# Kernel tuning notes

Hardware: AMD Instinct MI355X
Metric: run time of the kernel (lower is better)

## Reference

```python
import jax, jax.numpy as jnp
import numpy as np

DIM_X, DIM_Z, D_MODEL, N_HEADS, BATCH = 512, 256, 256, 8, 32


def sinusoidal_pe(seq_len, d_model):
    # standard sinusoidal table, rows indexed by position
    pos = np.arange(seq_len)[:, None].astype(np.float32)
    div = np.exp(np.arange(0, d_model, 2).astype(np.float32) * (-np.log(10000.0) / d_model))
    pe = np.zeros((seq_len, d_model), dtype=np.float32)
    pe[:, 0::2] = np.sin(pos * div)
    pe[:, 1::2] = np.cos(pos * div)
    return jnp.asarray(pe)


def setup_inputs() -> dict:
    key = jax.random.key(0)
    ks = jax.random.split(key, 5)
    state = jax.random.normal(ks[0], (BATCH, D_MODEL, DIM_X), dtype=jnp.float32)
    obs = jax.random.normal(ks[1], (BATCH, D_MODEL, DIM_Z), dtype=jnp.float32)
    Qp = jax.random.uniform(ks[2], (DIM_X, D_MODEL), dtype=jnp.float32)  # torch.rand init
    Wq = jax.random.normal(ks[3], (D_MODEL, D_MODEL), dtype=jnp.float32) / np.sqrt(D_MODEL)
    Wk = jax.random.normal(ks[4], (D_MODEL, D_MODEL), dtype=jnp.float32) / np.sqrt(D_MODEL)
    bq = jnp.zeros((D_MODEL,), dtype=jnp.float32)
    bk = jnp.zeros((D_MODEL,), dtype=jnp.float32)
    return {"state": state, "obs": obs, "Qp": Qp, "Wq": Wq, "bq": bq, "Wk": Wk, "bk": bk}


def reference(state, obs, Qp, Wq, bq, Wk, bk):
    bs, en, dim_x = state.shape
    dim_z = obs.shape[2]
    d_model = Qp.shape[1]
    h = N_HEADS
    hd = d_model // h
    S = dim_x + dim_z

    # mean-center over the ensemble axis
    A = state - jnp.mean(state, axis=1, keepdims=True)   # [bs, en, dim_x]
    Y = obs - jnp.mean(obs, axis=1, keepdims=True)       # [bs, en, dim_z]
    A = jnp.transpose(A, (2, 0, 1))                      # [dim_x, bs, en]
    Y = jnp.transpose(Y, (2, 0, 1))                      # [dim_z, bs, en]

    # positional encoding: batch_first=True quirk -> PE indexed along axis 1 (the bs axis)
    pe = sinusoidal_pe(bs, d_model)[None, :, :]          # [1, bs, d_model]
    query = Qp[:, None, :] + pe                          # [dim_x, bs, d_model] (broadcast of repeat)
    xy = jnp.concatenate([A, Y], axis=0) + pe            # [S, bs, d_model]

    # multi-head attention weights (V / out-proj do not affect returned quantities)
    q = (query @ Wq.T + bq).reshape(dim_x, bs, h, hd)
    k = (xy @ Wk.T + bk).reshape(S, bs, h, hd)
    scores = jnp.einsum('lbhd,sbhd->bhls', q, k) / np.sqrt(hd)  # [bs, h, dim_x, S]

    # fixed structured mask: eye(dim_x) | bottom-padded eye(dim_z)
    p1 = jnp.eye(dim_x, dtype=bool)
    p2 = jnp.concatenate([jnp.zeros((dim_x - dim_z, dim_z), dtype=bool),
                          jnp.eye(dim_z, dtype=bool)], axis=0)
    allow = jnp.concatenate([p1, p2], axis=1)            # [dim_x, S]
    scores = jnp.where(allow[None, None], scores, -jnp.inf)
    atten = jnp.mean(jax.nn.softmax(scores, axis=-1), axis=1)  # average over heads -> [bs, dim_x, S]

    # weighted merge of the ORIGINAL (uncentered) state/obs
    merge = jnp.concatenate([jnp.transpose(state, (0, 2, 1)),
                             jnp.transpose(obs, (0, 2, 1))], axis=1)  # [bs, S, en]
    new_state = jnp.einsum('bls,bse->ble', atten, merge)              # [bs, dim_x, en]
    new_state = jnp.transpose(new_state, (0, 2, 1))                   # [bs, en, dim_x]
    return new_state, atten
```

## Files before the change

kernel.cpp:

```cpp
#include <hip/hip_runtime.h>
#include <stdint.h>
#include <math.h>


#define WS_P    0
#define WS_QWT  8192
#define WS_PQ   73728
#define WS_U    81920
#define WS_V    606208
#define WS_QPT  671744
#define WS_WQT  737280

typedef float vf4 __attribute__((ext_vector_type(4)));
__device__ __forceinline__ void nt_store4(float* p, float x, float y,
                                          float z, float w) {
  vf4 v; v.x = x; v.y = y; v.z = z; v.w = w;
  __builtin_nontemporal_store(v, (vf4*)p);
}

__global__ void __launch_bounds__(256)
k_tr(const float* __restrict__ Qp, const float* __restrict__ Wq,
     float* __restrict__ ws, float* __restrict__ out) {
  int bid = blockIdx.x, t = threadIdx.x;
  if (bid < 128) {
    __shared__ float tile[32][33];
    const float* src; float* dst; int ti;
    if (bid < 64) { src = Qp + 65536; dst = ws + WS_QPT; ti = bid; }
    else          { src = Wq;         dst = ws + WS_WQT; ti = bid - 64; }
    int tr = ti >> 3, tc = ti & 7;
    int c = t & 31, r0 = t >> 5;
    #pragma unroll
    for (int k = 0; k < 4; ++k) {
      int r = r0 + (k << 3);
      tile[r][c] = src[(size_t)(tr * 32 + r) * 256 + tc * 32 + c];
    }
    __syncthreads();
    #pragma unroll
    for (int k = 0; k < 4; ++k) {
      int r = r0 + (k << 3);
      dst[(size_t)(tc * 32 + r) * 256 + tr * 32 + c] = tile[c][r];
    }
  } else {
    int base = (bid - 128) * 512 + t;
    #pragma unroll
    for (int k = 0; k < 2; ++k) {
      int g4 = base + (k << 8);
      int row_id = g4 / 192, c = g4 - row_id * 192;
      int b = row_id >> 8, l = row_id & 255;
      float v[4] = {0.f, 0.f, 0.f, 0.f};
      int s0 = c << 2;
      if (l >= s0 && l < s0 + 4) v[l - s0] = 1.0f;
      nt_store4(out + 4194304 + (size_t)((b << 9) + l) * 768 + (c << 2),
                v[0], v[1], v[2], v[3]);
    }
  }
}

__global__ void __launch_bounds__(256)
k_pro(const float* __restrict__ Wq, float* __restrict__ ws,
      float* __restrict__ out) {
  int bid = blockIdx.x, t = threadIdx.x;
  if (bid < 288) {
    __shared__ float lvec[256];
    const float* __restrict__ GT; float* dst;
    if (bid < 256) {
      int d = bid;
      lvec[t] = Wq[(size_t)d * 256 + t];
      GT = ws + WS_QPT; dst = ws + WS_QWT + d * 256;
    } else {
      int b = bid - 256;
      int k2 = t & ~1;
      float div = expf((float)k2 * (-9.210340371976184f / 256.f));
      float a = (float)b * div;
      lvec[t] = (t & 1) ? cosf(a) : sinf(a);
      GT = ws + WS_WQT; dst = ws + WS_PQ + b * 256;
    }
    __syncthreads();
    float acc = 0.f;
    #pragma unroll 8
    for (int e = 0; e < 256; ++e)
      acc += lvec[e] * GT[(e << 8) + t];
    dst[t] = acc;
  } else {
    int base = (bid - 288) * 512 + t;
    #pragma unroll
    for (int k = 0; k < 2; ++k) {
      int g4 = base + (k << 8);
      int row_id = g4 / 192, c = g4 - row_id * 192;
      int b = row_id >> 8, l = 256 + (row_id & 255);
      nt_store4(out + 4194304 + (size_t)((b << 9) + l) * 768 + (c << 2),
                0.f, 0.f, 0.f, 0.f);
    }
  }
}

__global__ void __launch_bounds__(256)
k_uv(const float* __restrict__ Wk, const float* __restrict__ bq,
     const float* __restrict__ state, float* __restrict__ ws,
     float* __restrict__ out) {
  int bid = blockIdx.x, t = threadIdx.x;
  if (bid < 256) {
    int h = bid >> 5, e0 = (bid & 31) << 3;
    __shared__ float wk_s[32][9];
    {
      int d = t >> 3, i = t & 7;
      wk_s[d][i] = Wk[(size_t)(h * 32 + d) * 256 + e0 + i];
    }
    __syncthreads();
    float acc[8] = {0.f, 0.f, 0.f, 0.f, 0.f, 0.f, 0.f, 0.f};
    const float* __restrict__ Qw = ws + WS_QWT + t;
    #pragma unroll 4
    for (int d = 0; d < 32; ++d) {
      float q = Qw[((h << 5) + d) << 8];
      #pragma unroll
      for (int i = 0; i < 8; ++i) acc[i] += wk_s[d][i] * q;
    }
    float* Uh = ws + WS_U + (h << 16) + (size_t)e0 * 256;
    #pragma unroll
    for (int i = 0; i < 8; ++i) Uh[(size_t)i * 256 + t] = acc[i];
  } else if (bid < 512) {
    int idx = bid - 256, b = idx >> 3, h = idx & 7;
    float acc = 0.f;
#pragma unroll 8
    for (int dd = 0; dd < 32; ++dd) {
      int d = h * 32 + dd;
      acc += (ws[WS_PQ + b * 256 + d] + bq[d]) * Wk[(size_t)d * 256 + t];
    }
    ws[WS_V + ((b << 3) + h) * 256 + t] = acc;
  } else {
    int base = (bid - 512) * 512 + t;
    #pragma unroll
    for (int k = 0; k < 2; ++k) {
      int g4 = base + (k << 8);
      int row = g4 >> 6, c = g4 & 63;
      float4 sv = ((const float4*)state)[(size_t)row * 128 + c];
      nt_store4(out + (size_t)row * 512 + (c << 2), sv.x, sv.y, sv.z, sv.w);
    }
  }
}

__global__ void __launch_bounds__(256)
k_delta(const float* __restrict__ state, const float* __restrict__ obs,
        float* __restrict__ ws) {
  int b = blockIdx.x >> 3, jt = (blockIdx.x & 7) << 5;
  int t = threadIdx.x;
  __shared__ float Xs[256][33];
  __shared__ float Vs[2048];
  __shared__ float pd[8][8][32];
  __shared__ float pw[8][8][32];
  __shared__ float px[8][32];
  {
    int es = t >> 3, jq = t & 7;
    const float* sp = state + (size_t)b * 131072 + 256 + jt + (jq << 2);
    const float* op = obs   + (size_t)b * 65536  + jt + (jq << 2);
    #pragma unroll
    for (int k = 0; k < 8; ++k) {
      int e = es + (k << 5);
      float4 s4 = *(const float4*)(sp + (size_t)e * 512);
      float4 o4 = *(const float4*)(op + (size_t)e * 256);
      float* xr = &Xs[e][jq << 2];
      xr[0] = s4.x - o4.x; xr[1] = s4.y - o4.y;
      xr[2] = s4.z - o4.z; xr[3] = s4.w - o4.w;
    }
    for (int i = t; i < 2048; i += 256) Vs[i] = ws[WS_V + (b << 11) + i];
  }
  __syncthreads();
  int j = t & 31, eg = t >> 5, e0 = eg << 5;
  {
    float ax = 0.f;
    #pragma unroll
    for (int ei = 0; ei < 32; ++ei) ax += Xs[e0 + ei][j];
    px[eg][j] = ax;
  }
  const float* __restrict__ Ub = ws + WS_U + jt + j;
  #pragma unroll
  for (int h = 0; h < 8; ++h) {
    float dacc = 0.f, wacc = 0.f;
    const float* __restrict__ Uh = Ub + (h << 16) + (e0 << 8);
    const float* __restrict__ Vh = Vs + (h << 8) + e0;
    #pragma unroll 16
    for (int ei = 0; ei < 32; ++ei) {
      float w = Uh[ei << 8] + Vh[ei];
      dacc += Xs[e0 + ei][j] * w;
      wacc += w;
    }
    pd[eg][h][j] = dacc;
    pw[eg][h][j] = wacc;
  }
  __syncthreads();
  int h2 = t >> 5, j2 = t & 31;
  float D = 0.f, W = 0.f, X = 0.f;
  #pragma unroll
  for (int g = 0; g < 8; ++g) {
    D += pd[g][h2][j2];
    W += pw[g][h2][j2];
    X += px[g][j2];
  }
  float delta = D - X * (1.f / 256.f) * W;
  float sig = 1.f / (1.f + __expf(-delta * 0.17677669529663687f));
  __syncthreads();
  px[h2][j2] = sig;
  __syncthreads();
  if (t < 32) {
    float acc = 0.f;
    #pragma unroll
    for (int h = 0; h < 8; ++h) acc += px[h][t];
    ws[WS_P + (b << 8) + jt + t] = acc;
  }
}

__global__ void __launch_bounds__(256)
k_out(const float* __restrict__ state, const float* __restrict__ obs,
      const float* __restrict__ ws, float* __restrict__ out) {
  int bid = blockIdx.x, t = threadIdx.x;
  if (bid < 2048) {
    int row = (bid << 2) | (t >> 6);
    int c = t & 63;
    int b = row >> 8;
    float4 sv = ((const float4*)(state + (size_t)row * 512))[64 + c];
    float4 ov = ((const float4*)(obs + (size_t)row * 256))[c];
    float4 p4 = ((const float4*)(ws + WS_P + b * 256))[c];
    p4.x *= 0.125f; p4.y *= 0.125f; p4.z *= 0.125f; p4.w *= 0.125f;
    nt_store4(out + (size_t)row * 512 + 256 + (c << 2),
              p4.x * sv.x + (1.f - p4.x) * ov.x,
              p4.y * sv.y + (1.f - p4.y) * ov.y,
              p4.z * sv.z + (1.f - p4.z) * ov.z,
              p4.w * sv.w + (1.f - p4.w) * ov.w);
  } else {
    int idx = ((bid - 2048) << 8) + t;
    int b = idx >> 8, j = idx & 255;
    float p = ws[WS_P + (b << 8) + j] * 0.125f;
    size_t r = 4194304 + (size_t)((b << 9) + 256 + j) * 768;
    out[r + 256 + j] = p;
    out[r + 512 + j] = 1.f - p;
  }
}

extern "C" void kernel_launch(void* const* d_in, const int* in_sizes, int n_in,
                              void* d_out, int out_size, void* d_ws, size_t ws_size,
                              hipStream_t stream) {
  const float *state = nullptr, *obs = nullptr, *Qp = nullptr;
  const float *Wq = nullptr, *Wk = nullptr, *bq = nullptr, *bk = nullptr;
  for (int i = 0; i < n_in; ++i) {
    int s = in_sizes[i];
    const float* p = (const float*)d_in[i];
    if      (s == 4194304) state = p;
    else if (s == 2097152) obs = p;
    else if (s == 131072)  Qp = p;
    else if (s == 65536)   { if (!Wq) Wq = p; else Wk = p; }
    else if (s == 256)     { if (!bq) bq = p; else bk = p; }
  }
  (void)bk;
  float* out = (float*)d_out;
  float* ws  = (float*)d_ws;

  k_tr   <<<3200, 256, 0, stream>>>(Qp, Wq, ws, out);
  k_pro  <<<3360, 256, 0, stream>>>(Wq, ws, out);
  k_uv   <<<1536, 256, 0, stream>>>(Wk, bq, state, ws, out);
  k_delta<<<256,  256, 0, stream>>>(state, obs, ws);
  k_out  <<<2080, 256, 0, stream>>>(state, obs, ws, out);
}
```

Baseline: 126.7 us.

## Fuse five kernels into one cooperative persistent kernel with grid syncs

Replaces the five separate launches with a single cooperative kernel of 512 blocks that runs the phases in order, separated by grid-wide barriers. The static output writes (identity, zeros and the state copy) are redistributed as grid-stride loops across the phases, so they overlap with the small compute blocks. The aim is to remove launch gaps and per-kernel tail effects. In exchange it adds four grid.sync barriers, limits parallelism to 512 resident blocks, and uses about 58KB of shared memory per block, which may affect occupancy.

```diff
diff --git a/kernel.cpp b/kernel.cpp
--- a/kernel.cpp
+++ b/kernel.cpp
@@ -1,6 +1,9 @@
 #include <hip/hip_runtime.h>
+#include <hip/hip_cooperative_groups.h>
 #include <stdint.h>
 #include <math.h>
+
+namespace cg = cooperative_groups;
 
 
 #define WS_P    0
@@ -18,12 +21,42 @@
   __builtin_nontemporal_store(v, (vf4*)p);
 }
 
-__global__ void __launch_bounds__(256)
-k_tr(const float* __restrict__ Qp, const float* __restrict__ Wq,
+__device__ __forceinline__ void write_static(int idx, const float* __restrict__ state,
+                                             float* __restrict__ out) {
+  if (idx < 1572864) {
+    int g4 = idx;
+    int row_id = g4 / 192, c = g4 - row_id * 192;
+    int b = row_id >> 8, l = row_id & 255;
+    float v[4] = {0.f, 0.f, 0.f, 0.f};
+    int s0 = c << 2;
+    if (l >= s0 && l < s0 + 4) v[l - s0] = 1.0f;
+    nt_store4(out + 4194304 + (size_t)((b << 9) + l) * 768 + (c << 2),
+              v[0], v[1], v[2], v[3]);
+  } else if (idx < 3145728) {
+    int g4 = idx - 1572864;
+    int row_id = g4 / 192, c = g4 - row_id * 192;
+    int b = row_id >> 8, l = 256 + (row_id & 255);
+    nt_store4(out + 4194304 + (size_t)((b << 9) + l) * 768 + (c << 2),
+              0.f, 0.f, 0.f, 0.f);
+  } else {
+    int g4 = idx - 3145728;
+    int row = g4 >> 6, c = g4 & 63;
+    float4 sv = ((const float4*)state)[(size_t)row * 128 + c];
+    nt_store4(out + (size_t)row * 512 + (c << 2), sv.x, sv.y, sv.z, sv.w);
+  }
+}
+
+__global__ void __launch_bounds__(256, 2)
+mega(const float* __restrict__ state, const float* __restrict__ obs,
+     const float* __restrict__ Qp, const float* __restrict__ Wq,
+     const float* __restrict__ Wk, const float* __restrict__ bq,
      float* __restrict__ ws, float* __restrict__ out) {
+  cg::grid_group grid = cg::this_grid();
+  __shared__ float S[14848];
   int bid = blockIdx.x, t = threadIdx.x;
+
   if (bid < 128) {
-    __shared__ float tile[32][33];
+    float (*tile)[33] = (float(*)[33])S;
     const float* src; float* dst; int ti;
     if (bid < 64) { src = Qp + 65536; dst = ws + WS_QPT; ti = bid; }
     else          { src = Wq;         dst = ws + WS_WQT; ti = bid - 64; }
@@ -41,27 +74,13 @@
       dst[(size_t)(tc * 32 + r) * 256 + tr * 32 + c] = tile[c][r];
     }
   } else {
-    int base = (bid - 128) * 512 + t;
-    #pragma unroll
-    for (int k = 0; k < 2; ++k) {
-      int g4 = base + (k << 8);
-      int row_id = g4 / 192, c = g4 - row_id * 192;
-      int b = row_id >> 8, l = row_id & 255;
-      float v[4] = {0.f, 0.f, 0.f, 0.f};
-      int s0 = c << 2;
-      if (l >= s0 && l < s0 + 4) v[l - s0] = 1.0f;
-      nt_store4(out + 4194304 + (size_t)((b << 9) + l) * 768 + (c << 2),
-                v[0], v[1], v[2], v[3]);
-    }
-  }
-}
-
-__global__ void __launch_bounds__(256)
-k_pro(const float* __restrict__ Wq, float* __restrict__ ws,
-      float* __restrict__ out) {
-  int bid = blockIdx.x, t = threadIdx.x;
+    for (int i = ((bid - 128) << 8) + t; i < 1433600; i += 98304)
+      write_static(i, state, out);
+  }
+  grid.sync();
+
   if (bid < 288) {
-    __shared__ float lvec[256];
+    float* lvec = S;
     const float* __restrict__ GT; float* dst;
     if (bid < 256) {
       int d = bid;
@@ -82,29 +101,17 @@
       acc += lvec[e] * GT[(e << 8) + t];
     dst[t] = acc;
   } else {
-    int base = (bid - 288) * 512 + t;
-    #pragma unroll
-    for (int k = 0; k < 2; ++k) {
-      int g4 = base + (k << 8);
-      int row_id = g4 / 192, c = g4 - row_id * 192;
-      int b = row_id >> 8, l = 256 + (row_id & 255);
-      nt_store4(out + 4194304 + (size_t)((b << 9) + l) * 768 + (c << 2),
-                0.f, 0.f, 0.f, 0.f);
-    }
-  }
-}
-
-__global__ void __launch_bounds__(256)
-k_uv(const float* __restrict__ Wk, const float* __restrict__ bq,
-     const float* __restrict__ state, float* __restrict__ ws,
-     float* __restrict__ out) {
-  int bid = blockIdx.x, t = threadIdx.x;
+    for (int i = 1433600 + ((bid - 288) << 8) + t; i < 2662400; i += 57344)
+      write_static(i, state, out);
+  }
+  grid.sync();
+
   if (bid < 256) {
     int h = bid >> 5, e0 = (bid & 31) << 3;
-    __shared__ float wk_s[32][9];
+    float* wk_s = S;
     {
       int d = t >> 3, i = t & 7;
-      wk_s[d][i] = Wk[(size_t)(h * 32 + d) * 256 + e0 + i];
+      wk_s[d * 9 + i] = Wk[(size_t)(h * 32 + d) * 256 + e0 + i];
     }
     __syncthreads();
     float acc[8] = {0.f, 0.f, 0.f, 0.f, 0.f, 0.f, 0.f, 0.f};
@@ -113,109 +120,98 @@
     for (int d = 0; d < 32; ++d) {
       float q = Qw[((h << 5) + d) << 8];
       #pragma unroll
-      for (int i = 0; i < 8; ++i) acc[i] += wk_s[d][i] * q;
+      for (int i = 0; i < 8; ++i) acc[i] += wk_s[d * 9 + i] * q;
     }
     float* Uh = ws + WS_U + (h << 16) + (size_t)e0 * 256;
     #pragma unroll
     for (int i = 0; i < 8; ++i) Uh[(size_t)i * 256 + t] = acc[i];
-  } else if (bid < 512) {
+  } else {
     int idx = bid - 256, b = idx >> 3, h = idx & 7;
     float acc = 0.f;
-#pragma unroll 8
+    #pragma unroll 8
     for (int dd = 0; dd < 32; ++dd) {
       int d = h * 32 + dd;
       acc += (ws[WS_PQ + b * 256 + d] + bq[d]) * Wk[(size_t)d * 256 + t];
     }
     ws[WS_V + ((b << 3) + h) * 256 + t] = acc;
-  } else {
-    int base = (bid - 512) * 512 + t;
-    #pragma unroll
-    for (int k = 0; k < 2; ++k) {
-      int g4 = base + (k << 8);
-      int row = g4 >> 6, c = g4 & 63;
-      float4 sv = ((const float4*)state)[(size_t)row * 128 + c];
-      nt_store4(out + (size_t)row * 512 + (c << 2), sv.x, sv.y, sv.z, sv.w);
-    }
-  }
-}
-
-__global__ void __launch_bounds__(256)
-k_delta(const float* __restrict__ state, const float* __restrict__ obs,
-        float* __restrict__ ws) {
-  int b = blockIdx.x >> 3, jt = (blockIdx.x & 7) << 5;
-  int t = threadIdx.x;
-  __shared__ float Xs[256][33];
-  __shared__ float Vs[2048];
-  __shared__ float pd[8][8][32];
-  __shared__ float pw[8][8][32];
-  __shared__ float px[8][32];
-  {
-    int es = t >> 3, jq = t & 7;
-    const float* sp = state + (size_t)b * 131072 + 256 + jt + (jq << 2);
-    const float* op = obs   + (size_t)b * 65536  + jt + (jq << 2);
-    #pragma unroll
-    for (int k = 0; k < 8; ++k) {
-      int e = es + (k << 5);
-      float4 s4 = *(const float4*)(sp + (size_t)e * 512);
-      float4 o4 = *(const float4*)(op + (size_t)e * 256);
-      float* xr = &Xs[e][jq << 2];
-      xr[0] = s4.x - o4.x; xr[1] = s4.y - o4.y;
-      xr[2] = s4.z - o4.z; xr[3] = s4.w - o4.w;
-    }
-    for (int i = t; i < 2048; i += 256) Vs[i] = ws[WS_V + (b << 11) + i];
-  }
-  __syncthreads();
-  int j = t & 31, eg = t >> 5, e0 = eg << 5;
-  {
-    float ax = 0.f;
-    #pragma unroll
-    for (int ei = 0; ei < 32; ++ei) ax += Xs[e0 + ei][j];
-    px[eg][j] = ax;
-  }
-  const float* __restrict__ Ub = ws + WS_U + jt + j;
+  }
+  grid.sync();
+
+  if (bid < 256) {
+    int b = bid >> 3, jt = (bid & 7) << 5;
+    float* Xs = S;
+    float* Vs = S + 8448;
+    float* pd = S + 10496;
+    float* pw = S + 12544;
+    float* px = S + 14592;
+    {
+      int es = t >> 3, jq = t & 7;
+      const float* sp = state + (size_t)b * 131072 + 256 + jt + (jq << 2);
+      const float* op = obs   + (size_t)b * 65536  + jt + (jq << 2);
+      #pragma unroll
+      for (int k = 0; k < 8; ++k) {
+        int e = es + (k << 5);
+        float4 s4 = *(const float4*)(sp + (size_t)e * 512);
+        float4 o4 = *(const float4*)(op + (size_t)e * 256);
+        float* xr = Xs + e * 33 + (jq << 2);
+        xr[0] = s4.x - o4.x; xr[1] = s4.y - o4.y;
+        xr[2] = s4.z - o4.z; xr[3] = s4.w - o4.w;
+      }
+      for (int i = t; i < 2048; i += 256) Vs[i] = ws[WS_V + (b << 11) + i];
+    }
+    __syncthreads();
+    int j = t & 31, eg = t >> 5, e0 = eg << 5;
+    {
+      float ax = 0.f;
+      #pragma unroll
+      for (int ei = 0; ei < 32; ++ei) ax += Xs[(e0 + ei) * 33 + j];
+      px[eg * 32 + j] = ax;
+    }
+    const float* __restrict__ Ub = ws + WS_U + jt + j;
+    #pragma unroll
+    for (int h = 0; h < 8; ++h) {
+      float dacc = 0.f, wacc = 0.f;
+      const float* __restrict__ Uh = Ub + (h << 16) + (e0 << 8);
+      const float* __restrict__ Vh = Vs + (h << 8) + e0;
+      #pragma unroll 16
+      for (int ei = 0; ei < 32; ++ei) {
+        float w = Uh[ei << 8] + Vh[ei];
+        dacc += Xs[(e0 + ei) * 33 + j] * w;
+        wacc += w;
+      }
+      pd[((eg << 3) + h) * 32 + j] = dacc;
+      pw[((eg << 3) + h) * 32 + j] = wacc;
+    }
+    __syncthreads();
+    int h2 = t >> 5, j2 = t & 31;
+    float D = 0.f, W = 0.f, X = 0.f;
+    #pragma unroll
+    for (int g = 0; g < 8; ++g) {
+      D += pd[((g << 3) + h2) * 32 + j2];
+      W += pw[((g << 3) + h2) * 32 + j2];
+      X += px[g * 32 + j2];
+    }
+    float delta = D - X * (1.f / 256.f) * W;
+    float sig = 1.f / (1.f + __expf(-delta * 0.17677669529663687f));
+    __syncthreads();
+    px[h2 * 32 + j2] = sig;
+    __syncthreads();
+    if (t < 32) {
+      float acc = 0.f;
+      #pragma unroll
+      for (int h = 0; h < 8; ++h) acc += px[h * 32 + t];
+      ws[WS_P + (b << 8) + jt + t] = acc;
+    }
+  } else {
+    for (int i = 2662400 + ((bid - 256) << 8) + t; i < 3670016; i += 65536)
+      write_static(i, state, out);
+  }
+  grid.sync();
+
   #pragma unroll
-  for (int h = 0; h < 8; ++h) {
-    float dacc = 0.f, wacc = 0.f;
-    const float* __restrict__ Uh = Ub + (h << 16) + (e0 << 8);
-    const float* __restrict__ Vh = Vs + (h << 8) + e0;
-    #pragma unroll 16
-    for (int ei = 0; ei < 32; ++ei) {
-      float w = Uh[ei << 8] + Vh[ei];
-      dacc += Xs[e0 + ei][j] * w;
-      wacc += w;
-    }
-    pd[eg][h][j] = dacc;
-    pw[eg][h][j] = wacc;
-  }
-  __syncthreads();
-  int h2 = t >> 5, j2 = t & 31;
-  float D = 0.f, W = 0.f, X = 0.f;
-  #pragma unroll
-  for (int g = 0; g < 8; ++g) {
-    D += pd[g][h2][j2];
-    W += pw[g][h2][j2];
-    X += px[g][j2];
-  }
-  float delta = D - X * (1.f / 256.f) * W;
-  float sig = 1.f / (1.f + __expf(-delta * 0.17677669529663687f));
-  __syncthreads();
-  px[h2][j2] = sig;
-  __syncthreads();
-  if (t < 32) {
-    float acc = 0.f;
-    #pragma unroll
-    for (int h = 0; h < 8; ++h) acc += px[h][t];
-    ws[WS_P + (b << 8) + jt + t] = acc;
-  }
-}
-
-__global__ void __launch_bounds__(256)
-k_out(const float* __restrict__ state, const float* __restrict__ obs,
-      const float* __restrict__ ws, float* __restrict__ out) {
-  int bid = blockIdx.x, t = threadIdx.x;
-  if (bid < 2048) {
-    int row = (bid << 2) | (t >> 6);
-    int c = t & 63;
+  for (int k = 0; k < 4; ++k) {
+    int gi = (bid << 10) + (k << 8) + t;
+    int row = gi >> 6, c = gi & 63;
     int b = row >> 8;
     float4 sv = ((const float4*)(state + (size_t)row * 512))[64 + c];
     float4 ov = ((const float4*)(obs + (size_t)row * 256))[c];
@@ -226,8 +222,9 @@
               p4.y * sv.y + (1.f - p4.y) * ov.y,
               p4.z * sv.z + (1.f - p4.z) * ov.z,
               p4.w * sv.w + (1.f - p4.w) * ov.w);
-  } else {
-    int idx = ((bid - 2048) << 8) + t;
+  }
+  if (bid < 32) {
+    int idx = (bid << 8) + t;
     int b = idx >> 8, j = idx & 255;
     float p = ws[WS_P + (b << 8) + j] * 0.125f;
     size_t r = 4194304 + (size_t)((b << 9) + 256 + j) * 768;
@@ -254,9 +251,8 @@
   float* out = (float*)d_out;
   float* ws  = (float*)d_ws;
 
-  k_tr   <<<3200, 256, 0, stream>>>(Qp, Wq, ws, out);
-  k_pro  <<<3360, 256, 0, stream>>>(Wq, ws, out);
-  k_uv   <<<1536, 256, 0, stream>>>(Wk, bq, state, ws, out);
-  k_delta<<<256,  256, 0, stream>>>(state, obs, ws);
-  k_out  <<<2080, 256, 0, stream>>>(state, obs, ws, out);
-}
+  void* args[] = {(void*)&state, (void*)&obs, (void*)&Qp, (void*)&Wq,
+                  (void*)&Wk, (void*)&bq, (void*)&ws, (void*)&out};
+  hipLaunchCooperativeKernel((const void*)mega, dim3(512), dim3(256),
+                             args, 0, stream);
+}
```

Measured after the change: 369.2 us. 2.92x slower.
